# Performance work log

Hardware: AMD Instinct MI355X
Metric: run time of the kernel (lower is better)

The kernel has to match this reference:

```python
import jax, jax.numpy as jnp
import numpy as np

CH, XH, YH, RADIUS = 2, 2, 2, 1  # channel_heads, x_heads, y_heads, neighborhood radius


def neighborhood_mask(n_sub_x, n_sub_y, radius):
    # clamped neighbor offsets reduce to |di|<=r and |dj|<=r within the grid
    iy = jnp.arange(n_sub_y)
    ix = jnp.arange(n_sub_x)
    my = jnp.abs(iy[:, None] - iy[None, :]) <= radius  # [ny, ny]
    mx = jnp.abs(ix[:, None] - ix[None, :]) <= radius  # [nx, nx]
    m = my[:, None, :, None] & mx[None, :, None, :]    # [ny, nx, ny, nx]
    s = n_sub_x * n_sub_y
    return m.reshape(s, s)  # row-major (h1 w1)(h2 w2), matching einops


def setup_inputs() -> dict:
    key = jax.random.key(0)
    k1, k2, k3 = jax.random.split(key, 3)
    C = 128
    seq = jax.random.normal(k1, (2, 256, C, 16, 16), dtype=jnp.float32)
    w_qkv = jax.random.normal(k2, (3 * C, C), dtype=jnp.float32) / np.sqrt(C).astype(np.float32)
    w_out = jax.random.normal(k3, (C, C), dtype=jnp.float32) / np.sqrt(C).astype(np.float32)
    b_out = jnp.zeros((C,), dtype=jnp.float32)
    return {"seq": seq, "w_qkv": w_qkv, "w_out": w_out, "b_out": b_out,
            "n_sub_x": 16, "n_sub_y": 16}


def reference(seq, w_qkv, w_out, b_out, n_sub_x, n_sub_y):
    b, s, C, H, W = seq.shape
    h, w = H // YH, W // XH
    c = C // CH
    nH = YH * XH * CH  # total heads

    # pointwise qkv projection over channels: [b, s, 3C, H, W]
    qkv = jnp.einsum('bschw,dc->bsdhw', seq, w_qkv)

    # decompose2d: split spatial grid into y_heads x x_heads blocks -> spatial heads
    # [b, s, 3C, YH, h, XH, w] -> [b, s, YH*XH, 3C, h, w]
    qkv = qkv.reshape(b, s, 3 * C, YH, h, XH, w)
    qkv = qkv.transpose(0, 1, 3, 5, 2, 4, 6).reshape(b, s, YH * XH, 3 * C, h, w)

    # split into q,k,v and channel heads: 3C = 3 * CH * c
    qkv = qkv.reshape(b, s, YH * XH, 3, CH, c, h, w)
    # -> [3, b, (spatial_heads * channel_heads), s, c, h, w]
    qkv = qkv.transpose(3, 0, 2, 4, 1, 5, 6, 7).reshape(3, b, nH, s, c, h, w)
    q, k, v = qkv[0], qkv[1], qkv[2]

    # scaled dot-product attention over flattened function dim (c,h,w)
    scale = 1.0 / np.sqrt(c * h * w).astype(np.float32)
    scores = jnp.einsum('bnschw,bntchw->bnst', q, k) * scale  # [b, nH, s, s]
    mask = neighborhood_mask(n_sub_x, n_sub_y, RADIUS)  # [s, s]
    scores = jnp.where(mask[None, None, :, :], scores, jnp.finfo(scores.dtype).min)
    attn = jax.nn.softmax(scores, axis=-1)
    sa = jnp.einsum('bnst,bntchw->bnschw', attn, v)  # [b, nH, s, c, h, w]

    # merge channel heads back: [b, s, spatial_heads, C, h, w]
    sa = sa.reshape(b, YH * XH, CH, s, c, h, w)
    sa = sa.transpose(0, 3, 1, 2, 4, 5, 6).reshape(b, s, YH, XH, C, h, w)
    # recompose2d: [b, s, C, H, W]
    sa = sa.transpose(0, 1, 4, 2, 5, 3, 6).reshape(b, s, C, H, W)

    # output pointwise projection with bias
    out = jnp.einsum('bschw,dc->bsdhw', sa, w_out) + b_out[None, None, :, None, None]
    return out
```

## Files before the change

### kernel.cpp

```cpp
#include <hip/hip_runtime.h>

#define BATCH 2
#define SS    256
#define CC    128
#define HWN   256
#define FDIM  4096

typedef unsigned int uint;
typedef unsigned short ushort;
typedef short bf16x8 __attribute__((ext_vector_type(8)));
typedef ushort us4 __attribute__((ext_vector_type(4)));
typedef float f32x4 __attribute__((ext_vector_type(4)));

__device__ __forceinline__ ushort f2b(float f) {
  uint u = __float_as_uint(f);
  return (ushort)((u + 0x7fffu + ((u >> 16) & 1u)) >> 16);
}
__device__ __forceinline__ float b2f(ushort h) { return __uint_as_float((uint)h << 16); }

__global__ __launch_bounds__(512, 4) void k_qkv(const float* __restrict__ seq,
                                                const float* __restrict__ wqkv,
                                                ushort* __restrict__ qkvh) {
  __shared__ ushort wlds[128 * 128];
  const int bs = blockIdx.x;
  const int b = bs >> 8, s = bs & 255;
  const int t = threadIdx.x;
  const int wv = t >> 6, lane = t & 63;
  const int qq = lane >> 4, m = lane & 15;

  const float* sp = seq + (size_t)bs * (CC * HWN);

  bf16x8 bfrag[2][4];
  uint obase[2];
  #pragma unroll
  for (int set = 0; set < 2; ++set) {
    const int ntg = wv * 2 + set;
    const int hw = ntg * 16 + m;
    #pragma unroll
    for (int ks = 0; ks < 4; ++ks) {
      const int k0 = ks * 32 + qq * 8;
      float tmp[8];
      #pragma unroll
      for (int j = 0; j < 8; ++j) tmp[j] = sp[(k0 + j) * HWN + hw];
      bf16x8 fr;
      #pragma unroll
      for (int j = 0; j < 8; ++j) fr[j] = (short)f2b(tmp[j]);
      bfrag[set][ks] = fr;
    }
    const int n_qk = ((ntg >> 3) * 2 + (m >> 3)) * 2;
    const int hwl  = (ntg & 7) * 8 + (m & 7);
    obase[set] = (uint)(((b * 8 + n_qk) * SS + s) * FDIM + hwl * 16 + qq * 4);
  }

  for (int qkvi = 0; qkvi < 3; ++qkvi) {
    if (qkvi) __syncthreads();
    #pragma unroll
    for (int i = 0; i < 4; ++i) {
      const int row = i * 32 + (t >> 4), col16 = t & 15;
      const float* wp = wqkv + (size_t)(qkvi * 128 + row) * 128 + col16 * 8;
      f32x4 w0 = *(const f32x4*)(wp);
      f32x4 w1 = *(const f32x4*)(wp + 4);
      bf16x8 fr;
      #pragma unroll
      for (int e = 0; e < 4; ++e) { fr[e] = (short)f2b(w0[e]); fr[4 + e] = (short)f2b(w1[e]); }
      *(bf16x8*)&wlds[row * 128 + ((col16 ^ (row & 15)) * 8)] = fr;
    }
    __syncthreads();

    #pragma unroll
    for (int mt8 = 0; mt8 < 8; ++mt8) {
      bf16x8 afrag[4];
      #pragma unroll
      for (int ks = 0; ks < 4; ++ks)
        afrag[ks] = *(const bf16x8*)&wlds[(mt8 * 16 + m) * 128 + (((ks * 4 + qq) ^ m) * 8)];
      const int ch = mt8 >> 2, m4 = mt8 & 3;
      #pragma unroll
      for (int set = 0; set < 2; ++set) {
        f32x4 acc = {0.f, 0.f, 0.f, 0.f};
        #pragma unroll
        for (int ks = 0; ks < 4; ++ks)
          acc = __builtin_amdgcn_mfma_f32_16x16x32_bf16(afrag[ks], bfrag[set][ks], acc, 0, 0, 0);
        us4 pk;
        #pragma unroll
        for (int r = 0; r < 4; ++r) pk[r] = f2b(acc[r]);
        *(us4*)(qkvh + obase[set]
                + (uint)((qkvi * 16 + ch) * (SS * FDIM) + m4 * 1024)) = pk;
      }
    }
  }
}

__global__ __launch_bounds__(1024) void k_scores(const ushort* __restrict__ qkvh,
                                                 float* __restrict__ attn) {
  __shared__ float red[16][64][12];
  const int g = blockIdx.x;
  const int unit = (g & 7) * 32 + (g >> 3);
  const int b  = unit >> 7;
  const int n  = (unit >> 4) & 7;
  const int sy = unit & 15;
  const int t = threadIdx.x;
  const int wave = t >> 6, lane = t & 63;
  const int qq = lane >> 4, l15 = lane & 15;
  const size_t hs = (size_t)SS * FDIM;
  const ushort* qb = qkvh + (size_t)(b * 8 + n) * hs;
  const ushort* kb = qkvh + (size_t)(16 + b * 8 + n) * hs;

  const ushort* qp = qb + (size_t)(sy * 16 + l15) * FDIM + qq * 8;
  const ushort* kp[3];
  #pragma unroll
  for (int tl = 0; tl < 3; ++tl) {
    const int tyc = min(max(sy - 1 + tl, 0), 15);
    kp[tl] = kb + (size_t)(tyc * 16 + l15) * FDIM + qq * 8;
  }

  f32x4 acc[3] = {{0,0,0,0},{0,0,0,0},{0,0,0,0}};
  const int kbeg = wave * 256;
  #pragma unroll
  for (int it = 0; it < 4; ++it) {
    const int k0 = kbeg + it * 64;
    bf16x8 a0 = *(const bf16x8*)(qp + k0);
    bf16x8 a1 = *(const bf16x8*)(qp + k0 + 32);
    bf16x8 b0[3], b1[3];
    #pragma unroll
    for (int tl = 0; tl < 3; ++tl) {
      b0[tl] = *(const bf16x8*)(kp[tl] + k0);
      b1[tl] = *(const bf16x8*)(kp[tl] + k0 + 32);
    }
    #pragma unroll
    for (int tl = 0; tl < 3; ++tl)
      acc[tl] = __builtin_amdgcn_mfma_f32_16x16x32_bf16(a0, b0[tl], acc[tl], 0, 0, 0);
    #pragma unroll
    for (int tl = 0; tl < 3; ++tl)
      acc[tl] = __builtin_amdgcn_mfma_f32_16x16x32_bf16(a1, b1[tl], acc[tl], 0, 0, 0);
  }

  #pragma unroll
  for (int tl = 0; tl < 3; ++tl)
    #pragma unroll
    for (int r = 0; r < 4; ++r) red[wave][lane][tl * 4 + r] = acc[tl][r];
  __syncthreads();
  if (t < 768) {
    const int lane2 = t / 12, idx = t - lane2 * 12;
    float ssum = red[0][lane2][idx];
    #pragma unroll
    for (int w = 1; w < 16; ++w) ssum += red[w][lane2][idx];
    red[0][lane2][idx] = ssum;
  }
  __syncthreads();
  if (wave != 0) return;
  #pragma unroll
  for (int tl = 0; tl < 3; ++tl)
    #pragma unroll
    for (int r = 0; r < 4; ++r) acc[tl][r] = red[0][lane][tl * 4 + r];

  const int tx = l15;
  float sc[3][4];
  #pragma unroll
  for (int tl = 0; tl < 3; ++tl) {
    const int ty = sy - 1 + tl;
    const bool tyv = (ty >= 0 && ty < 16);
    #pragma unroll
    for (int r = 0; r < 4; ++r) {
      const int sx = qq * 4 + r;
      const bool v = tyv && (tx - sx <= 1) && (sx - tx <= 1);
      sc[tl][r] = v ? acc[tl][r] * (1.f / 64.f) : -1e30f;
    }
  }
  #pragma unroll
  for (int r = 0; r < 4; ++r) {
    float mx = fmaxf(fmaxf(sc[0][r], sc[1][r]), sc[2][r]);
    #pragma unroll
    for (int off = 1; off < 16; off <<= 1) mx = fmaxf(mx, __shfl_xor(mx, off));
    float p[3], sum = 0.f;
    #pragma unroll
    for (int tl = 0; tl < 3; ++tl) { p[tl] = __expf(sc[tl][r] - mx); sum += p[tl]; }
    #pragma unroll
    for (int off = 1; off < 16; off <<= 1) sum += __shfl_xor(sum, off);
    const float inv = 1.f / sum;
    const int sx = qq * 4 + r;
    const int s = sy * 16 + sx;
    #pragma unroll
    for (int tl = 0; tl < 3; ++tl) {
      const int ty = sy - 1 + tl;
      const int dxp = tx - sx + 1;
      if (ty >= 0 && ty < 16 && dxp >= 0 && dxp <= 2)
        attn[((size_t)(b * 8 + n) * SS + s) * 9 + tl * 3 + dxp] = p[tl] * inv;
    }
  }
}

__global__ __launch_bounds__(256) void k_out(const ushort* __restrict__ qkvh,
                                             const float* __restrict__ attn,
                                             const float* __restrict__ wout,
                                             const float* __restrict__ bout,
                                             float* __restrict__ out) {
  __shared__ ushort wlds[128 * 128];
  const int g = blockIdx.x;
  const int r9 = g >> 3;
  const int G = (g & 7) * 4 + (r9 >> 6);
  const int idx = r9 & 63;
  const int b = G >> 4, sy = G & 15;
  const int sx = idx >> 2, sub = idx & 3;
  const int s = sy * 16 + sx;
  const int bs = b * 256 + s;
  const int t = threadIdx.x;
  const int wave = t >> 6, lane = t & 63;
  const int ntg = sub * 4 + wave;
  const int qq = lane >> 4, m = lane & 15;
  const size_t hs = (size_t)SS * FDIM;

  {
    const int col16 = t & 15;
    const int ks = col16 >> 2, qw = col16 & 3;
    const int creal0 = (ks >> 1) * 64 + ((((ks & 1) << 1) | (qw >> 1)) << 4)
                       + ((qw & 1) << 3);
    #pragma unroll
    for (int i = 0; i < 8; ++i) {
      const int row = i * 16 + (t >> 4);
      const float* wp = wout + (size_t)row * 128 + creal0;
      f32x4 w0 = *(const f32x4*)(wp);
      f32x4 w1 = *(const f32x4*)(wp + 4);
      bf16x8 fr;
      #pragma unroll
      for (int e = 0; e < 4; ++e) { fr[e] = (short)f2b(w0[e]); fr[4 + e] = (short)f2b(w1[e]); }
      *(bf16x8*)&wlds[row * 128 + ((col16 ^ (row & 15)) * 8)] = fr;
    }
  }

  int sjc[9];
  bool vld[9];
  #pragma unroll
  for (int j = 0; j < 9; ++j) {
    const int ny = sy + j / 3 - 1, nx = sx + j % 3 - 1;
    vld[j] = (ny >= 0 && ny < 16 && nx >= 0 && nx < 16);
    sjc[j] = min(max(ny, 0), 15) * 16 + min(max(nx, 0), 15);
  }

  const int nbase = ((ntg >> 3) * 2 + (m >> 3)) * 2;
  float pch[2][9];
  #pragma unroll
  for (int ch = 0; ch < 2; ++ch) {
    #pragma unroll
    for (int j = 0; j < 9; ++j) {
      const float w = attn[((size_t)(b * 8 + nbase + ch) * SS + s) * 9 + j];
      pch[ch][j] = vld[j] ? w : 0.f;
    }
  }

  const int hwl = (ntg & 7) * 8 + (m & 7);
  bf16x8 bfrag[4];
  #pragma unroll
  for (int ks = 0; ks < 4; ++ks) {
    const int ch = ks >> 1;
    const int c64hi = ((ks & 1) << 1) | (qq >> 1);
    const int half = qq & 1;
    const ushort* vb = qkvh + (size_t)(32 + b * 8 + nbase + ch) * hs;
    const int off = c64hi * 1024 + hwl * 16 + half * 8;
    float facc[8] = {0.f, 0.f, 0.f, 0.f, 0.f, 0.f, 0.f, 0.f};
    #pragma unroll
    for (int j = 0; j < 9; ++j) {
      bf16x8 vv = *(const bf16x8*)(vb + (size_t)sjc[j] * FDIM + off);
      const float pj = pch[ch][j];
      #pragma unroll
      for (int e = 0; e < 8; ++e) facc[e] += pj * b2f((ushort)vv[e]);
    }
    bf16x8 fr;
    #pragma unroll
    for (int e = 0; e < 8; ++e) fr[e] = (short)f2b(facc[e]);
    bfrag[ks] = fr;
  }

  __syncthreads();

  #pragma unroll
  for (int mt = 0; mt < 8; ++mt) {
    bf16x8 afrag[4];
    #pragma unroll
    for (int ks = 0; ks < 4; ++ks)
      afrag[ks] = *(const bf16x8*)&wlds[(mt * 16 + m) * 128 + (((ks * 4 + qq) ^ m) * 8)];
    f32x4 acc = {0.f, 0.f, 0.f, 0.f};
    #pragma unroll
    for (int ks = 0; ks < 4; ++ks)
      acc = __builtin_amdgcn_mfma_f32_16x16x32_bf16(afrag[ks], bfrag[ks], acc, 0, 0, 0);
    const int hw = ntg * 16 + m;
    #pragma unroll
    for (int r = 0; r < 4; ++r) {
      const int d = mt * 16 + qq * 4 + r;
      out[((size_t)bs * CC + d) * HWN + hw] = acc[r] + bout[d];
    }
  }
}

extern "C" void kernel_launch(void* const* d_in, const int* in_sizes, int n_in,
                              void* d_out, int out_size, void* d_ws, size_t ws_size,
                              hipStream_t stream) {
  const float* seq  = (const float*)d_in[0];
  const float* wqkv = (const float*)d_in[1];
  const float* wout = (const float*)d_in[2];
  const float* bout = (const float*)d_in[3];
  char* ws = (char*)d_ws;
  ushort* qkvh = (ushort*)(ws);
  float*  attn = (float*)(ws + 100663296ull);
  float*  outp = (float*)d_out;

  hipLaunchKernelGGL(k_qkv,    dim3(512),  dim3(512),  0, stream, seq, wqkv, qkvh);
  hipLaunchKernelGGL(k_scores, dim3(256),  dim3(1024), 0, stream, qkvh, attn);
  hipLaunchKernelGGL(k_out,    dim3(2048), dim3(256),  0, stream, qkvh, attn, wout, bout, outp);
}
```

Baseline: 188.4 us.

## Fuse qkv, scores and output kernels into one cooperative persistent kernel

Merges the three separate launches into a single cooperative kernel of 256 blocks of 1024 threads, with grid-wide syncs between the QKV projection, the score/softmax and the attention-apply/output-projection phases. Each block now handles two sequence positions in the QKV phase and eight output units in the final phase. The aim is to remove launch gaps and kernel-boundary drain. In exchange the grid shrinks to 256 large blocks, which may reduce occupancy and latency hiding in the memory-bound phases, and the grid syncs add their own cost.

After: 421.2 us. +123.6%, slower.

```diff
diff --git a/kernel.cpp b/kernel.cpp
--- a/kernel.cpp
+++ b/kernel.cpp
@@ -1,4 +1,5 @@
 #include <hip/hip_runtime.h>
+#include <hip/hip_cooperative_groups.h>
 
 #define BATCH 2
 #define SS    256
@@ -18,275 +19,284 @@
 }
 __device__ __forceinline__ float b2f(ushort h) { return __uint_as_float((uint)h << 16); }
 
-__global__ __launch_bounds__(512, 4) void k_qkv(const float* __restrict__ seq,
-                                                const float* __restrict__ wqkv,
-                                                ushort* __restrict__ qkvh) {
-  __shared__ ushort wlds[128 * 128];
-  const int bs = blockIdx.x;
-  const int b = bs >> 8, s = bs & 255;
+__global__ __launch_bounds__(1024, 4) void k_fused(const float* __restrict__ seq,
+                                                   const float* __restrict__ wqkv,
+                                                   const float* __restrict__ wout,
+                                                   const float* __restrict__ bout,
+                                                   ushort* __restrict__ qkvh,
+                                                   float* __restrict__ attn,
+                                                   float* __restrict__ out) {
+  __shared__ char smem[49152];
+  ushort* wlds = (ushort*)smem;
+  float (*red)[64][12] = (float (*)[64][12])smem;
+
   const int t = threadIdx.x;
-  const int wv = t >> 6, lane = t & 63;
-  const int qq = lane >> 4, m = lane & 15;
-
-  const float* sp = seq + (size_t)bs * (CC * HWN);
-
-  bf16x8 bfrag[2][4];
-  uint obase[2];
-  #pragma unroll
-  for (int set = 0; set < 2; ++set) {
-    const int ntg = wv * 2 + set;
-    const int hw = ntg * 16 + m;
+  const int blk = blockIdx.x;
+  const size_t hs = (size_t)SS * FDIM;
+
+  {
+    const int h  = t >> 9;
+    const int bs = blk * 2 + h;
+    const int b = bs >> 8, s = bs & 255;
+    const int wv = (t >> 6) & 7;
+    const int lane = t & 63;
+    const int qq = lane >> 4, m = lane & 15;
+
+    const float* sp = seq + (size_t)bs * (CC * HWN);
+
+    bf16x8 bfrag[2][4];
+    uint obase[2];
     #pragma unroll
-    for (int ks = 0; ks < 4; ++ks) {
-      const int k0 = ks * 32 + qq * 8;
-      float tmp[8];
-      #pragma unroll
-      for (int j = 0; j < 8; ++j) tmp[j] = sp[(k0 + j) * HWN + hw];
-      bf16x8 fr;
-      #pragma unroll
-      for (int j = 0; j < 8; ++j) fr[j] = (short)f2b(tmp[j]);
-      bfrag[set][ks] = fr;
-    }
-    const int n_qk = ((ntg >> 3) * 2 + (m >> 3)) * 2;
-    const int hwl  = (ntg & 7) * 8 + (m & 7);
-    obase[set] = (uint)(((b * 8 + n_qk) * SS + s) * FDIM + hwl * 16 + qq * 4);
+    for (int set = 0; set < 2; ++set) {
+      const int ntg = wv * 2 + set;
+      const int hw = ntg * 16 + m;
+      #pragma unroll
+      for (int ks = 0; ks < 4; ++ks) {
+        const int k0 = ks * 32 + qq * 8;
+        float tmp[8];
+        #pragma unroll
+        for (int j = 0; j < 8; ++j) tmp[j] = sp[(k0 + j) * HWN + hw];
+        bf16x8 fr;
+        #pragma unroll
+        for (int j = 0; j < 8; ++j) fr[j] = (short)f2b(tmp[j]);
+        bfrag[set][ks] = fr;
+      }
+      const int n_qk = ((ntg >> 3) * 2 + (m >> 3)) * 2;
+      const int hwl  = (ntg & 7) * 8 + (m & 7);
+      obase[set] = (uint)(((b * 8 + n_qk) * SS + s) * FDIM + hwl * 16 + qq * 4);
+    }
+
+    for (int qkvi = 0; qkvi < 3; ++qkvi) {
+      if (qkvi) __syncthreads();
+      #pragma unroll
+      for (int i = 0; i < 2; ++i) {
+        const int row = i * 64 + (t >> 4), col16 = t & 15;
+        const float* wp = wqkv + (size_t)(qkvi * 128 + row) * 128 + col16 * 8;
+        f32x4 w0 = *(const f32x4*)(wp);
+        f32x4 w1 = *(const f32x4*)(wp + 4);
+        bf16x8 fr;
+        #pragma unroll
+        for (int e = 0; e < 4; ++e) { fr[e] = (short)f2b(w0[e]); fr[4 + e] = (short)f2b(w1[e]); }
+        *(bf16x8*)&wlds[row * 128 + ((col16 ^ (row & 15)) * 8)] = fr;
+      }
+      __syncthreads();
+
+      #pragma unroll
+      for (int mt8 = 0; mt8 < 8; ++mt8) {
+        bf16x8 afrag[4];
+        #pragma unroll
+        for (int ks = 0; ks < 4; ++ks)
+          afrag[ks] = *(const bf16x8*)&wlds[(mt8 * 16 + m) * 128 + (((ks * 4 + qq) ^ m) * 8)];
+        const int ch = mt8 >> 2, m4 = mt8 & 3;
+        #pragma unroll
+        for (int set = 0; set < 2; ++set) {
+          f32x4 acc = {0.f, 0.f, 0.f, 0.f};
+          #pragma unroll
+          for (int ks = 0; ks < 4; ++ks)
+            acc = __builtin_amdgcn_mfma_f32_16x16x32_bf16(afrag[ks], bfrag[set][ks], acc, 0, 0, 0);
+          us4 pk;
+          #pragma unroll
+          for (int r = 0; r < 4; ++r) pk[r] = f2b(acc[r]);
+          *(us4*)(qkvh + obase[set]
+                  + (uint)((qkvi * 16 + ch) * (SS * FDIM) + m4 * 1024)) = pk;
+        }
+      }
+    }
   }
 
-  for (int qkvi = 0; qkvi < 3; ++qkvi) {
-    if (qkvi) __syncthreads();
-    #pragma unroll
-    for (int i = 0; i < 4; ++i) {
-      const int row = i * 32 + (t >> 4), col16 = t & 15;
-      const float* wp = wqkv + (size_t)(qkvi * 128 + row) * 128 + col16 * 8;
-      f32x4 w0 = *(const f32x4*)(wp);
-      f32x4 w1 = *(const f32x4*)(wp + 4);
-      bf16x8 fr;
-      #pragma unroll
-      for (int e = 0; e < 4; ++e) { fr[e] = (short)f2b(w0[e]); fr[4 + e] = (short)f2b(w1[e]); }
-      *(bf16x8*)&wlds[row * 128 + ((col16 ^ (row & 15)) * 8)] = fr;
-    }
-    __syncthreads();
-
-    #pragma unroll
-    for (int mt8 = 0; mt8 < 8; ++mt8) {
-      bf16x8 afrag[4];
-      #pragma unroll
-      for (int ks = 0; ks < 4; ++ks)
-        afrag[ks] = *(const bf16x8*)&wlds[(mt8 * 16 + m) * 128 + (((ks * 4 + qq) ^ m) * 8)];
-      const int ch = mt8 >> 2, m4 = mt8 & 3;
-      #pragma unroll
-      for (int set = 0; set < 2; ++set) {
-        f32x4 acc = {0.f, 0.f, 0.f, 0.f};
-        #pragma unroll
-        for (int ks = 0; ks < 4; ++ks)
-          acc = __builtin_amdgcn_mfma_f32_16x16x32_bf16(afrag[ks], bfrag[set][ks], acc, 0, 0, 0);
-        us4 pk;
-        #pragma unroll
-        for (int r = 0; r < 4; ++r) pk[r] = f2b(acc[r]);
-        *(us4*)(qkvh + obase[set]
-                + (uint)((qkvi * 16 + ch) * (SS * FDIM) + m4 * 1024)) = pk;
-      }
-    }
-  }
-}
-
-__global__ __launch_bounds__(1024) void k_scores(const ushort* __restrict__ qkvh,
-                                                 float* __restrict__ attn) {
-  __shared__ float red[16][64][12];
-  const int g = blockIdx.x;
-  const int unit = (g & 7) * 32 + (g >> 3);
-  const int b  = unit >> 7;
-  const int n  = (unit >> 4) & 7;
-  const int sy = unit & 15;
-  const int t = threadIdx.x;
-  const int wave = t >> 6, lane = t & 63;
-  const int qq = lane >> 4, l15 = lane & 15;
-  const size_t hs = (size_t)SS * FDIM;
-  const ushort* qb = qkvh + (size_t)(b * 8 + n) * hs;
-  const ushort* kb = qkvh + (size_t)(16 + b * 8 + n) * hs;
-
-  const ushort* qp = qb + (size_t)(sy * 16 + l15) * FDIM + qq * 8;
-  const ushort* kp[3];
-  #pragma unroll
-  for (int tl = 0; tl < 3; ++tl) {
-    const int tyc = min(max(sy - 1 + tl, 0), 15);
-    kp[tl] = kb + (size_t)(tyc * 16 + l15) * FDIM + qq * 8;
-  }
-
-  f32x4 acc[3] = {{0,0,0,0},{0,0,0,0},{0,0,0,0}};
-  const int kbeg = wave * 256;
-  #pragma unroll
-  for (int it = 0; it < 4; ++it) {
-    const int k0 = kbeg + it * 64;
-    bf16x8 a0 = *(const bf16x8*)(qp + k0);
-    bf16x8 a1 = *(const bf16x8*)(qp + k0 + 32);
-    bf16x8 b0[3], b1[3];
+  cooperative_groups::this_grid().sync();
+
+  {
+    const int unit = (blk & 7) * 32 + (blk >> 3);
+    const int b  = unit >> 7;
+    const int n  = (unit >> 4) & 7;
+    const int sy = unit & 15;
+    const int wave = t >> 6, lane = t & 63;
+    const int qq = lane >> 4, l15 = lane & 15;
+    const ushort* qb = qkvh + (size_t)(b * 8 + n) * hs;
+    const ushort* kb = qkvh + (size_t)(16 + b * 8 + n) * hs;
+
+    const ushort* qp = qb + (size_t)(sy * 16 + l15) * FDIM + qq * 8;
+    const ushort* kp[3];
     #pragma unroll
     for (int tl = 0; tl < 3; ++tl) {
-      b0[tl] = *(const bf16x8*)(kp[tl] + k0);
-      b1[tl] = *(const bf16x8*)(kp[tl] + k0 + 32);
-    }
+      const int tyc = min(max(sy - 1 + tl, 0), 15);
+      kp[tl] = kb + (size_t)(tyc * 16 + l15) * FDIM + qq * 8;
+    }
+
+    f32x4 acc[3] = {{0,0,0,0},{0,0,0,0},{0,0,0,0}};
+    const int kbeg = wave * 256;
+    #pragma unroll
+    for (int it = 0; it < 4; ++it) {
+      const int k0 = kbeg + it * 64;
+      bf16x8 a0 = *(const bf16x8*)(qp + k0);
+      bf16x8 a1 = *(const bf16x8*)(qp + k0 + 32);
+      bf16x8 b0[3], b1[3];
+      #pragma unroll
+      for (int tl = 0; tl < 3; ++tl) {
+        b0[tl] = *(const bf16x8*)(kp[tl] + k0);
+        b1[tl] = *(const bf16x8*)(kp[tl] + k0 + 32);
+      }
+      #pragma unroll
+      for (int tl = 0; tl < 3; ++tl)
+        acc[tl] = __builtin_amdgcn_mfma_f32_16x16x32_bf16(a0, b0[tl], acc[tl], 0, 0, 0);
+      #pragma unroll
+      for (int tl = 0; tl < 3; ++tl)
+        acc[tl] = __builtin_amdgcn_mfma_f32_16x16x32_bf16(a1, b1[tl], acc[tl], 0, 0, 0);
+    }
+
     #pragma unroll
     for (int tl = 0; tl < 3; ++tl)
-      acc[tl] = __builtin_amdgcn_mfma_f32_16x16x32_bf16(a0, b0[tl], acc[tl], 0, 0, 0);
-    #pragma unroll
-    for (int tl = 0; tl < 3; ++tl)
-      acc[tl] = __builtin_amdgcn_mfma_f32_16x16x32_bf16(a1, b1[tl], acc[tl], 0, 0, 0);
+      #pragma unroll
+      for (int r = 0; r < 4; ++r) red[wave][lane][tl * 4 + r] = acc[tl][r];
+    __syncthreads();
+    if (t < 768) {
+      const int lane2 = t / 12, idx = t - lane2 * 12;
+      float ssum = red[0][lane2][idx];
+      #pragma unroll
+      for (int w = 1; w < 16; ++w) ssum += red[w][lane2][idx];
+      red[0][lane2][idx] = ssum;
+    }
+    __syncthreads();
+    if (wave == 0) {
+      #pragma unroll
+      for (int tl = 0; tl < 3; ++tl)
+        #pragma unroll
+        for (int r = 0; r < 4; ++r) acc[tl][r] = red[0][lane][tl * 4 + r];
+
+      const int tx = l15;
+      float sc[3][4];
+      #pragma unroll
+      for (int tl = 0; tl < 3; ++tl) {
+        const int ty = sy - 1 + tl;
+        const bool tyv = (ty >= 0 && ty < 16);
+        #pragma unroll
+        for (int r = 0; r < 4; ++r) {
+          const int sx = qq * 4 + r;
+          const bool v = tyv && (tx - sx <= 1) && (sx - tx <= 1);
+          sc[tl][r] = v ? acc[tl][r] * (1.f / 64.f) : -1e30f;
+        }
+      }
+      #pragma unroll
+      for (int r = 0; r < 4; ++r) {
+        float mx = fmaxf(fmaxf(sc[0][r], sc[1][r]), sc[2][r]);
+        #pragma unroll
+        for (int off = 1; off < 16; off <<= 1) mx = fmaxf(mx, __shfl_xor(mx, off));
+        float p[3], sum = 0.f;
+        #pragma unroll
+        for (int tl = 0; tl < 3; ++tl) { p[tl] = __expf(sc[tl][r] - mx); sum += p[tl]; }
+        #pragma unroll
+        for (int off = 1; off < 16; off <<= 1) sum += __shfl_xor(sum, off);
+        const float inv = 1.f / sum;
+        const int sx = qq * 4 + r;
+        const int s = sy * 16 + sx;
+        #pragma unroll
+        for (int tl = 0; tl < 3; ++tl) {
+          const int ty = sy - 1 + tl;
+          const int dxp = tx - sx + 1;
+          if (ty >= 0 && ty < 16 && dxp >= 0 && dxp <= 2)
+            attn[((size_t)(b * 8 + n) * SS + s) * 9 + tl * 3 + dxp] = p[tl] * inv;
+        }
+      }
+    }
   }
 
-  #pragma unroll
-  for (int tl = 0; tl < 3; ++tl)
-    #pragma unroll
-    for (int r = 0; r < 4; ++r) red[wave][lane][tl * 4 + r] = acc[tl][r];
-  __syncthreads();
-  if (t < 768) {
-    const int lane2 = t / 12, idx = t - lane2 * 12;
-    float ssum = red[0][lane2][idx];
-    #pragma unroll
-    for (int w = 1; w < 16; ++w) ssum += red[w][lane2][idx];
-    red[0][lane2][idx] = ssum;
-  }
-  __syncthreads();
-  if (wave != 0) return;
-  #pragma unroll
-  for (int tl = 0; tl < 3; ++tl)
-    #pragma unroll
-    for (int r = 0; r < 4; ++r) acc[tl][r] = red[0][lane][tl * 4 + r];
-
-  const int tx = l15;
-  float sc[3][4];
-  #pragma unroll
-  for (int tl = 0; tl < 3; ++tl) {
-    const int ty = sy - 1 + tl;
-    const bool tyv = (ty >= 0 && ty < 16);
-    #pragma unroll
-    for (int r = 0; r < 4; ++r) {
-      const int sx = qq * 4 + r;
-      const bool v = tyv && (tx - sx <= 1) && (sx - tx <= 1);
-      sc[tl][r] = v ? acc[tl][r] * (1.f / 64.f) : -1e30f;
-    }
-  }
-  #pragma unroll
-  for (int r = 0; r < 4; ++r) {
-    float mx = fmaxf(fmaxf(sc[0][r], sc[1][r]), sc[2][r]);
-    #pragma unroll
-    for (int off = 1; off < 16; off <<= 1) mx = fmaxf(mx, __shfl_xor(mx, off));
-    float p[3], sum = 0.f;
-    #pragma unroll
-    for (int tl = 0; tl < 3; ++tl) { p[tl] = __expf(sc[tl][r] - mx); sum += p[tl]; }
-    #pragma unroll
-    for (int off = 1; off < 16; off <<= 1) sum += __shfl_xor(sum, off);
-    const float inv = 1.f / sum;
-    const int sx = qq * 4 + r;
-    const int s = sy * 16 + sx;
-    #pragma unroll
-    for (int tl = 0; tl < 3; ++tl) {
-      const int ty = sy - 1 + tl;
-      const int dxp = tx - sx + 1;
-      if (ty >= 0 && ty < 16 && dxp >= 0 && dxp <= 2)
-        attn[((size_t)(b * 8 + n) * SS + s) * 9 + tl * 3 + dxp] = p[tl] * inv;
-    }
-  }
-}
-
-__global__ __launch_bounds__(256) void k_out(const ushort* __restrict__ qkvh,
-                                             const float* __restrict__ attn,
-                                             const float* __restrict__ wout,
-                                             const float* __restrict__ bout,
-                                             float* __restrict__ out) {
-  __shared__ ushort wlds[128 * 128];
-  const int g = blockIdx.x;
-  const int r9 = g >> 3;
-  const int G = (g & 7) * 4 + (r9 >> 6);
-  const int idx = r9 & 63;
-  const int b = G >> 4, sy = G & 15;
-  const int sx = idx >> 2, sub = idx & 3;
-  const int s = sy * 16 + sx;
-  const int bs = b * 256 + s;
-  const int t = threadIdx.x;
-  const int wave = t >> 6, lane = t & 63;
-  const int ntg = sub * 4 + wave;
-  const int qq = lane >> 4, m = lane & 15;
-  const size_t hs = (size_t)SS * FDIM;
+  cooperative_groups::this_grid().sync();
 
   {
-    const int col16 = t & 15;
-    const int ks = col16 >> 2, qw = col16 & 3;
-    const int creal0 = (ks >> 1) * 64 + ((((ks & 1) << 1) | (qw >> 1)) << 4)
-                       + ((qw & 1) << 3);
-    #pragma unroll
-    for (int i = 0; i < 8; ++i) {
-      const int row = i * 16 + (t >> 4);
-      const float* wp = wout + (size_t)row * 128 + creal0;
-      f32x4 w0 = *(const f32x4*)(wp);
-      f32x4 w1 = *(const f32x4*)(wp + 4);
-      bf16x8 fr;
-      #pragma unroll
-      for (int e = 0; e < 4; ++e) { fr[e] = (short)f2b(w0[e]); fr[4 + e] = (short)f2b(w1[e]); }
-      *(bf16x8*)&wlds[row * 128 + ((col16 ^ (row & 15)) * 8)] = fr;
-    }
-  }
-
-  int sjc[9];
-  bool vld[9];
-  #pragma unroll
-  for (int j = 0; j < 9; ++j) {
-    const int ny = sy + j / 3 - 1, nx = sx + j % 3 - 1;
-    vld[j] = (ny >= 0 && ny < 16 && nx >= 0 && nx < 16);
-    sjc[j] = min(max(ny, 0), 15) * 16 + min(max(nx, 0), 15);
-  }
-
-  const int nbase = ((ntg >> 3) * 2 + (m >> 3)) * 2;
-  float pch[2][9];
-  #pragma unroll
-  for (int ch = 0; ch < 2; ++ch) {
-    #pragma unroll
-    for (int j = 0; j < 9; ++j) {
-      const float w = attn[((size_t)(b * 8 + nbase + ch) * SS + s) * 9 + j];
-      pch[ch][j] = vld[j] ? w : 0.f;
-    }
-  }
-
-  const int hwl = (ntg & 7) * 8 + (m & 7);
-  bf16x8 bfrag[4];
-  #pragma unroll
-  for (int ks = 0; ks < 4; ++ks) {
-    const int ch = ks >> 1;
-    const int c64hi = ((ks & 1) << 1) | (qq >> 1);
-    const int half = qq & 1;
-    const ushort* vb = qkvh + (size_t)(32 + b * 8 + nbase + ch) * hs;
-    const int off = c64hi * 1024 + hwl * 16 + half * 8;
-    float facc[8] = {0.f, 0.f, 0.f, 0.f, 0.f, 0.f, 0.f, 0.f};
-    #pragma unroll
-    for (int j = 0; j < 9; ++j) {
-      bf16x8 vv = *(const bf16x8*)(vb + (size_t)sjc[j] * FDIM + off);
-      const float pj = pch[ch][j];
-      #pragma unroll
-      for (int e = 0; e < 8; ++e) facc[e] += pj * b2f((ushort)vv[e]);
-    }
-    bf16x8 fr;
-    #pragma unroll
-    for (int e = 0; e < 8; ++e) fr[e] = (short)f2b(facc[e]);
-    bfrag[ks] = fr;
-  }
-
-  __syncthreads();
-
-  #pragma unroll
-  for (int mt = 0; mt < 8; ++mt) {
-    bf16x8 afrag[4];
-    #pragma unroll
-    for (int ks = 0; ks < 4; ++ks)
-      afrag[ks] = *(const bf16x8*)&wlds[(mt * 16 + m) * 128 + (((ks * 4 + qq) ^ m) * 8)];
-    f32x4 acc = {0.f, 0.f, 0.f, 0.f};
-    #pragma unroll
-    for (int ks = 0; ks < 4; ++ks)
-      acc = __builtin_amdgcn_mfma_f32_16x16x32_bf16(afrag[ks], bfrag[ks], acc, 0, 0, 0);
-    const int hw = ntg * 16 + m;
-    #pragma unroll
-    for (int r = 0; r < 4; ++r) {
-      const int d = mt * 16 + qq * 4 + r;
-      out[((size_t)bs * CC + d) * HWN + hw] = acc[r] + bout[d];
+    const int unit = (blk & 7) * 32 + (blk >> 3);
+    const int G = unit >> 3, idxg = unit & 7;
+    const int b = G >> 4, sy = G & 15;
+    const int wave = t >> 6, lane = t & 63;
+    const int s4 = wave >> 2, owave = wave & 3;
+    const int qq = lane >> 4, m = lane & 15;
+
+    {
+      const int col16 = t & 15;
+      const int ks = col16 >> 2, qw = col16 & 3;
+      const int creal0 = (ks >> 1) * 64 + ((((ks & 1) << 1) | (qw >> 1)) << 4)
+                         + ((qw & 1) << 3);
+      #pragma unroll
+      for (int i = 0; i < 2; ++i) {
+        const int row = i * 64 + (t >> 4);
+        const float* wp = wout + (size_t)row * 128 + creal0;
+        f32x4 w0 = *(const f32x4*)(wp);
+        f32x4 w1 = *(const f32x4*)(wp + 4);
+        bf16x8 fr;
+        #pragma unroll
+        for (int e = 0; e < 4; ++e) { fr[e] = (short)f2b(w0[e]); fr[4 + e] = (short)f2b(w1[e]); }
+        *(bf16x8*)&wlds[row * 128 + ((col16 ^ (row & 15)) * 8)] = fr;
+      }
+    }
+    __syncthreads();
+
+    for (int r = 0; r < 2; ++r) {
+      const int idx = idxg * 8 + r * 4 + s4;
+      const int sx = idx >> 2, sub = idx & 3;
+      const int s = sy * 16 + sx;
+      const int bs = b * 256 + s;
+      const int ntg = sub * 4 + owave;
+
+      int sjc[9];
+      bool vld[9];
+      #pragma unroll
+      for (int j = 0; j < 9; ++j) {
+        const int ny = sy + j / 3 - 1, nx = sx + j % 3 - 1;
+        vld[j] = (ny >= 0 && ny < 16 && nx >= 0 && nx < 16);
+        sjc[j] = min(max(ny, 0), 15) * 16 + min(max(nx, 0), 15);
+      }
+
+      const int nbase = ((ntg >> 3) * 2 + (m >> 3)) * 2;
+      float pch[2][9];
+      #pragma unroll
+      for (int ch = 0; ch < 2; ++ch) {
+        #pragma unroll
+        for (int j = 0; j < 9; ++j) {
+          const float w = attn[((size_t)(b * 8 + nbase + ch) * SS + s) * 9 + j];
+          pch[ch][j] = vld[j] ? w : 0.f;
+        }
+      }
+
+      const int hwl = (ntg & 7) * 8 + (m & 7);
+      bf16x8 bfrag[4];
+      #pragma unroll
+      for (int ks = 0; ks < 4; ++ks) {
+        const int ch = ks >> 1;
+        const int c64hi = ((ks & 1) << 1) | (qq >> 1);
+        const int half = qq & 1;
+        const ushort* vb = qkvh + (size_t)(32 + b * 8 + nbase + ch) * hs;
+        const int off = c64hi * 1024 + hwl * 16 + half * 8;
+        float facc[8] = {0.f, 0.f, 0.f, 0.f, 0.f, 0.f, 0.f, 0.f};
+        #pragma unroll
+        for (int j = 0; j < 9; ++j) {
+          bf16x8 vv = *(const bf16x8*)(vb + (size_t)sjc[j] * FDIM + off);
+          const float pj = pch[ch][j];
+          #pragma unroll
+          for (int e = 0; e < 8; ++e) facc[e] += pj * b2f((ushort)vv[e]);
+        }
+        bf16x8 fr;
+        #pragma unroll
+        for (int e = 0; e < 8; ++e) fr[e] = (short)f2b(facc[e]);
+        bfrag[ks] = fr;
+      }
+
+      #pragma unroll
+      for (int mt = 0; mt < 8; ++mt) {
+        bf16x8 afrag[4];
+        #pragma unroll
+        for (int ks = 0; ks < 4; ++ks)
+          afrag[ks] = *(const bf16x8*)&wlds[(mt * 16 + m) * 128 + (((ks * 4 + qq) ^ m) * 8)];
+        f32x4 acc = {0.f, 0.f, 0.f, 0.f};
+        #pragma unroll
+        for (int ks = 0; ks < 4; ++ks)
+          acc = __builtin_amdgcn_mfma_f32_16x16x32_bf16(afrag[ks], bfrag[ks], acc, 0, 0, 0);
+        const int hw = ntg * 16 + m;
+        #pragma unroll
+        for (int rr = 0; rr < 4; ++rr) {
+          const int d = mt * 16 + qq * 4 + rr;
+          out[((size_t)bs * CC + d) * HWN + hw] = acc[rr] + bout[d];
+        }
+      }
     }
   }
 }
@@ -303,7 +313,8 @@
   float*  attn = (float*)(ws + 100663296ull);
   float*  outp = (float*)d_out;
 
-  hipLaunchKernelGGL(k_qkv,    dim3(512),  dim3(512),  0, stream, seq, wqkv, qkvh);
-  hipLaunchKernelGGL(k_scores, dim3(256),  dim3(1024), 0, stream, qkvh, attn);
-  hipLaunchKernelGGL(k_out,    dim3(2048), dim3(256),  0, stream, qkvh, attn, wout, bout, outp);
+  void* args[] = { (void*)&seq, (void*)&wqkv, (void*)&wout, (void*)&bout,
+                   (void*)&qkvh, (void*)&attn, (void*)&outp };
+  hipLaunchCooperativeKernel((const void*)k_fused, dim3(256), dim3(1024),
+                             args, 0, stream);
 }
```

## Interleave Q/K storage by sub-row so score loads coalesce; swizzle qkv block order

Applied to the files above, without the earlier changes.

Q and K are now stored in a layout where the 16 sequence positions of one sub-grid row sit interleaved in 8-element chunks along the feature dimension. Each 16-lane MFMA fragment load in the scores kernel then reads one contiguous 256-byte span instead of 16 rows strided by the full feature size. The V layout is unchanged. The qkv kernel's block index is also remapped across groups of 8, probably to spread consecutive blocks over XCDs, and its Q/K stores become more scattered as a result.

Result: slower. 199.9 us (+6.1%).

```diff
diff --git a/kernel.cpp b/kernel.cpp
--- a/kernel.cpp
+++ b/kernel.cpp
@@ -5,6 +5,7 @@
 #define CC    128
 #define HWN   256
 #define FDIM  4096
+#define HS    (SS * FDIM)
 
 typedef unsigned int uint;
 typedef unsigned short ushort;
@@ -22,8 +23,10 @@
                                                 const float* __restrict__ wqkv,
                                                 ushort* __restrict__ qkvh) {
   __shared__ ushort wlds[128 * 128];
-  const int bs = blockIdx.x;
+  const int g = blockIdx.x;
+  const int bs = (g & 7) * 64 + (g >> 3);
   const int b = bs >> 8, s = bs & 255;
+  const int sy = s >> 4, sx = s & 15;
   const int t = threadIdx.x;
   const int wv = t >> 6, lane = t & 63;
   const int qq = lane >> 4, m = lane & 15;
@@ -31,7 +34,7 @@
   const float* sp = seq + (size_t)bs * (CC * HWN);
 
   bf16x8 bfrag[2][4];
-  uint obase[2];
+  uint oq[2], ov[2];
   #pragma unroll
   for (int set = 0; set < 2; ++set) {
     const int ntg = wv * 2 + set;
@@ -49,7 +52,9 @@
     }
     const int n_qk = ((ntg >> 3) * 2 + (m >> 3)) * 2;
     const int hwl  = (ntg & 7) * 8 + (m & 7);
-    obase[set] = (uint)(((b * 8 + n_qk) * SS + s) * FDIM + hwl * 16 + qq * 4);
+    ov[set] = (uint)(((b * 8 + n_qk) * SS + s) * FDIM + hwl * 16 + qq * 4);
+    oq[set] = (uint)((b * 8 + n_qk) * HS + sy * 65536 + hwl * 256
+                     + (qq >> 1) * 128 + sx * 8 + (qq & 1) * 4);
   }
 
   for (int qkvi = 0; qkvi < 3; ++qkvi) {
@@ -83,8 +88,10 @@
         us4 pk;
         #pragma unroll
         for (int r = 0; r < 4; ++r) pk[r] = f2b(acc[r]);
-        *(us4*)(qkvh + obase[set]
-                + (uint)((qkvi * 16 + ch) * (SS * FDIM) + m4 * 1024)) = pk;
+        const uint off = (qkvi < 2)
+            ? oq[set] + (uint)((qkvi * 16 + ch) * HS + m4 * 16384)
+            : ov[set] + (uint)((32 + ch) * HS + m4 * 1024);
+        *(us4*)(qkvh + off) = pk;
       }
     }
   }
@@ -101,16 +108,15 @@
   const int t = threadIdx.x;
   const int wave = t >> 6, lane = t & 63;
   const int qq = lane >> 4, l15 = lane & 15;
-  const size_t hs = (size_t)SS * FDIM;
-  const ushort* qb = qkvh + (size_t)(b * 8 + n) * hs;
-  const ushort* kb = qkvh + (size_t)(16 + b * 8 + n) * hs;
-
-  const ushort* qp = qb + (size_t)(sy * 16 + l15) * FDIM + qq * 8;
+  const ushort* qb = qkvh + (size_t)(b * 8 + n) * HS;
+  const ushort* kb = qkvh + (size_t)(16 + b * 8 + n) * HS;
+
+  const ushort* qp = qb + sy * 65536 + qq * 128 + l15 * 8;
   const ushort* kp[3];
   #pragma unroll
   for (int tl = 0; tl < 3; ++tl) {
     const int tyc = min(max(sy - 1 + tl, 0), 15);
-    kp[tl] = kb + (size_t)(tyc * 16 + l15) * FDIM + qq * 8;
+    kp[tl] = kb + tyc * 65536 + qq * 128 + l15 * 8;
   }
 
   f32x4 acc[3] = {{0,0,0,0},{0,0,0,0},{0,0,0,0}};
@@ -118,13 +124,14 @@
   #pragma unroll
   for (int it = 0; it < 4; ++it) {
     const int k0 = kbeg + it * 64;
-    bf16x8 a0 = *(const bf16x8*)(qp + k0);
-    bf16x8 a1 = *(const bf16x8*)(qp + k0 + 32);
+    const int koff = k0 * 16;
+    bf16x8 a0 = *(const bf16x8*)(qp + koff);
+    bf16x8 a1 = *(const bf16x8*)(qp + koff + 512);
     bf16x8 b0[3], b1[3];
     #pragma unroll
     for (int tl = 0; tl < 3; ++tl) {
-      b0[tl] = *(const bf16x8*)(kp[tl] + k0);
-      b1[tl] = *(const bf16x8*)(kp[tl] + k0 + 32);
+      b0[tl] = *(const bf16x8*)(kp[tl] + koff);
+      b1[tl] = *(const bf16x8*)(kp[tl] + koff + 512);
     }
     #pragma unroll
     for (int tl = 0; tl < 3; ++tl)
@@ -207,7 +214,6 @@
   const int wave = t >> 6, lane = t & 63;
   const int ntg = sub * 4 + wave;
   const int qq = lane >> 4, m = lane & 15;
-  const size_t hs = (size_t)SS * FDIM;
 
   {
     const int col16 = t & 15;
@@ -254,7 +260,7 @@
     const int ch = ks >> 1;
     const int c64hi = ((ks & 1) << 1) | (qq >> 1);
     const int half = qq & 1;
-    const ushort* vb = qkvh + (size_t)(32 + b * 8 + nbase + ch) * hs;
+    const ushort* vb = qkvh + (size_t)(32 + b * 8 + nbase + ch) * HS;
     const int off = c64hi * 1024 + hwl * 16 + half * 8;
     float facc[8] = {0.f, 0.f, 0.f, 0.f, 0.f, 0.f, 0.f, 0.f};
     #pragma unroll
```

## Stage Q/K rows through double-buffered swizzled LDS in k_scores with 256 threads

Applied to the files above, without the earlier changes.

k_scores now uses 4 waves per block instead of 16. All threads cooperatively copy the Q row and the three neighbor K row bands into a double-buffered, XOR-swizzled shared buffer in 256-element chunks, prefetching the next chunk while one wave runs MFMAs on the current one. The cross-wave reduction shrinks from 16 partials to 4, summed directly by wave 0. The intent is coalesced, overlapped global loads in place of strided per-lane loads. In exchange only one wave computes per chunk, which serializes the MFMA work and adds 16 block barriers.

Result: slower. 193.0 us (+2.5%).

```diff
diff --git a/kernel.cpp b/kernel.cpp
--- a/kernel.cpp
+++ b/kernel.cpp
@@ -90,9 +90,10 @@
   }
 }
 
-__global__ __launch_bounds__(1024) void k_scores(const ushort* __restrict__ qkvh,
-                                                 float* __restrict__ attn) {
-  __shared__ float red[16][64][12];
+__global__ __launch_bounds__(256) void k_scores(const ushort* __restrict__ qkvh,
+                                                float* __restrict__ attn) {
+  __shared__ ushort sq[2][64 * 256];
+  __shared__ float red[4][64][12];
   const int g = blockIdx.x;
   const int unit = (g & 7) * 32 + (g >> 3);
   const int b  = unit >> 7;
@@ -105,33 +106,49 @@
   const ushort* qb = qkvh + (size_t)(b * 8 + n) * hs;
   const ushort* kb = qkvh + (size_t)(16 + b * 8 + n) * hs;
 
-  const ushort* qp = qb + (size_t)(sy * 16 + l15) * FDIM + qq * 8;
-  const ushort* kp[3];
-  #pragma unroll
-  for (int tl = 0; tl < 3; ++tl) {
-    const int tyc = min(max(sy - 1 + tl, 0), 15);
-    kp[tl] = kb + (size_t)(tyc * 16 + l15) * FDIM + qq * 8;
+  const int r0 = t >> 5, slot = t & 31;
+  const ushort* rowsrc[8];
+  uint dst[8];
+  #pragma unroll
+  for (int i = 0; i < 8; ++i) {
+    const int r = r0 + 8 * i;
+    const ushort* base = (r < 16)
+      ? qb + (size_t)(sy * 16 + r) * FDIM
+      : kb + (size_t)(min(max(sy - 1 + ((r - 16) >> 4), 0), 15) * 16 + (r & 15)) * FDIM;
+    rowsrc[i] = base + slot * 8;
+    dst[i] = (uint)(r * 512 + ((slot ^ (r & 7)) * 16));
   }
 
   f32x4 acc[3] = {{0,0,0,0},{0,0,0,0},{0,0,0,0}};
-  const int kbeg = wave * 256;
-  #pragma unroll
-  for (int it = 0; it < 4; ++it) {
-    const int k0 = kbeg + it * 64;
-    bf16x8 a0 = *(const bf16x8*)(qp + k0);
-    bf16x8 a1 = *(const bf16x8*)(qp + k0 + 32);
-    bf16x8 b0[3], b1[3];
-    #pragma unroll
-    for (int tl = 0; tl < 3; ++tl) {
-      b0[tl] = *(const bf16x8*)(kp[tl] + k0);
-      b1[tl] = *(const bf16x8*)(kp[tl] + k0 + 32);
-    }
-    #pragma unroll
-    for (int tl = 0; tl < 3; ++tl)
-      acc[tl] = __builtin_amdgcn_mfma_f32_16x16x32_bf16(a0, b0[tl], acc[tl], 0, 0, 0);
-    #pragma unroll
-    for (int tl = 0; tl < 3; ++tl)
-      acc[tl] = __builtin_amdgcn_mfma_f32_16x16x32_bf16(a1, b1[tl], acc[tl], 0, 0, 0);
+
+  #pragma unroll
+  for (int i = 0; i < 8; ++i)
+    *(bf16x8*)((char*)sq[0] + dst[i]) = *(const bf16x8*)(rowsrc[i]);
+  __syncthreads();
+
+  for (int c = 0; c < 16; ++c) {
+    const int buf = c & 1;
+    if (c < 15) {
+      #pragma unroll
+      for (int i = 0; i < 8; ++i)
+        *(bf16x8*)((char*)sq[buf ^ 1] + dst[i]) =
+            *(const bf16x8*)(rowsrc[i] + (c + 1) * 256);
+    }
+    if ((c >> 2) == wave) {
+      const char* base = (const char*)sq[buf];
+      #pragma unroll
+      for (int k = 0; k < 8; ++k) {
+        const int sl = k * 4 + qq;
+        bf16x8 a = *(const bf16x8*)(base + l15 * 512 + ((sl ^ (l15 & 7)) * 16));
+        #pragma unroll
+        for (int tl = 0; tl < 3; ++tl) {
+          const int r = 16 + tl * 16 + l15;
+          bf16x8 bb = *(const bf16x8*)(base + r * 512 + ((sl ^ (r & 7)) * 16));
+          acc[tl] = __builtin_amdgcn_mfma_f32_16x16x32_bf16(a, bb, acc[tl], 0, 0, 0);
+        }
+      }
+    }
+    __syncthreads();
   }
 
   #pragma unroll
@@ -139,19 +156,13 @@
     #pragma unroll
     for (int r = 0; r < 4; ++r) red[wave][lane][tl * 4 + r] = acc[tl][r];
   __syncthreads();
-  if (t < 768) {
-    const int lane2 = t / 12, idx = t - lane2 * 12;
-    float ssum = red[0][lane2][idx];
-    #pragma unroll
-    for (int w = 1; w < 16; ++w) ssum += red[w][lane2][idx];
-    red[0][lane2][idx] = ssum;
-  }
-  __syncthreads();
   if (wave != 0) return;
   #pragma unroll
   for (int tl = 0; tl < 3; ++tl)
     #pragma unroll
-    for (int r = 0; r < 4; ++r) acc[tl][r] = red[0][lane][tl * 4 + r];
+    for (int r = 0; r < 4; ++r)
+      acc[tl][r] = red[0][lane][tl * 4 + r] + red[1][lane][tl * 4 + r]
+                 + red[2][lane][tl * 4 + r] + red[3][lane][tl * 4 + r];
 
   const int tx = l15;
   float sc[3][4];
@@ -303,7 +314,7 @@
   float*  attn = (float*)(ws + 100663296ull);
   float*  outp = (float*)d_out;
 
-  hipLaunchKernelGGL(k_qkv,    dim3(512),  dim3(512),  0, stream, seq, wqkv, qkvh);
-  hipLaunchKernelGGL(k_scores, dim3(256),  dim3(1024), 0, stream, qkvh, attn);
-  hipLaunchKernelGGL(k_out,    dim3(2048), dim3(256),  0, stream, qkvh, attn, wout, bout, outp);
-}
+  hipLaunchKernelGGL(k_qkv,    dim3(512),  dim3(512), 0, stream, seq, wqkv, qkvh);
+  hipLaunchKernelGGL(k_scores, dim3(256),  dim3(256), 0, stream, qkvh, attn);
+  hipLaunchKernelGGL(k_out,    dim3(2048), dim3(256), 0, stream, qkvh, attn, wout, bout, outp);
+}
```
